# Optimization experiments

Measured on AMD Instinct MI355X. Metric: run time of the kernel, lower is better.

## Reference

```python
import jax, jax.numpy as jnp
import numpy as np

B, S, I, H, O = 32, 512, 512, 1024, 512

def setup_inputs() -> dict:
    key = jax.random.key(0)
    ks = jax.random.split(key, 11)
    sI = 1.0 / np.sqrt(I + H)
    sH = 1.0 / np.sqrt(H)
    return {
        "x": jax.random.normal(ks[0], (B, S, I), jnp.float32),
        "Wf_w": jax.random.normal(ks[1], (H, I + H), jnp.float32) * sI,
        "Wf_b": jax.random.normal(ks[2], (H,), jnp.float32) * sI,
        "Wi_w": jax.random.normal(ks[3], (H, I + H), jnp.float32) * sI,
        "Wi_b": jax.random.normal(ks[4], (H,), jnp.float32) * sI,
        "Wo_w": jax.random.normal(ks[5], (H, I + H), jnp.float32) * sI,
        "Wo_b": jax.random.normal(ks[6], (H,), jnp.float32) * sI,
        "Wc_w": jax.random.normal(ks[7], (H, I + H), jnp.float32) * sI,
        "Wc_b": jax.random.normal(ks[8], (H,), jnp.float32) * sI,
        "out_w": jax.random.normal(ks[9], (O, H), jnp.float32) * sH,
        "out_b": jax.random.normal(ks[10], (O,), jnp.float32) * sH,
    }

def reference(x, Wf_w, Wf_b, Wi_w, Wi_b, Wo_w, Wo_b, Wc_w, Wc_b, out_w, out_b):
    # Stack the 4 gate projections into one [4H, I+H] matmul per step (same math).
    W = jnp.concatenate([Wf_w, Wi_w, Wo_w, Wc_w], axis=0)          # [4H, I+H]
    b = jnp.concatenate([Wf_b, Wi_b, Wo_b, Wc_b], axis=0)          # [4H]
    Wx, Wh = W[:, :x.shape[-1]], W[:, x.shape[-1]:]                # split cat(x, h)
    # Precompute input contributions for all timesteps: [S, B, 4H]
    xg = jnp.einsum('bsi,gi->sbg', x, Wx) + b

    h0 = jnp.zeros((x.shape[0], Wh.shape[1]), x.dtype)
    c0 = jnp.zeros_like(h0)

    def step(carry, xg_t):
        h, c = carry
        g = xg_t + h @ Wh.T                                        # [B, 4H]
        f, i, o, chat = jnp.split(g, 4, axis=-1)
        f, i, o = jax.nn.sigmoid(f), jax.nn.sigmoid(i), jax.nn.sigmoid(o)
        c = f * c + i * jnp.tanh(chat)
        h = o * jnp.tanh(c)
        return (h, c), h

    (h_fin, c_fin), hs = jax.lax.scan(step, (h0, c0), xg)          # hs: [S, B, H]
    outputs = jnp.transpose(hs, (1, 0, 2))                         # [B, S, H]
    final = jnp.einsum('bsh,oh->bso', outputs, out_w) + out_b      # [B, S, O]
    return final, (h_fin, c_fin)
```

## Files before the change

kernel.cpp:

```cpp
#include <hip/hip_runtime.h>

typedef unsigned short u16;
typedef __attribute__((ext_vector_type(8))) short short8;
typedef __attribute__((ext_vector_type(4))) float f32x4;
typedef __attribute__((ext_vector_type(2))) float f32x2;

#define S_ 512
#define I_ 512
#define H_ 1024
#define B_ 32
#define G_ 4096
#define WROW 1536
#define CH_ 128
#define CHLOG_ 7
#define NREC 64
#define NWRK 192

__device__ __forceinline__ u16 f2b(float f){ union{float f;unsigned u;}c; c.f=f; unsigned u=c.u; return (u16)((u + 0x7FFFu + ((u>>16)&1u))>>16); }

__device__ __forceinline__ unsigned pk2(float a, float b){
  union{float f;unsigned u;} x, y; x.f=a; y.f=b;
  return (x.u>>16) | (y.u & 0xffff0000u);
}
__device__ __forceinline__ short8 cvt8(const float* __restrict__ p){
  f32x4 a = *(const f32x4*)p;
  f32x4 b = *(const f32x4*)(p+4);
  union{unsigned u[4]; short8 s;} r;
  r.u[0]=pk2(a[0],a[1]); r.u[1]=pk2(a[2],a[3]);
  r.u[2]=pk2(b[0],b[1]); r.u[3]=pk2(b[2],b[3]);
  return r.s;
}
__device__ __forceinline__ short8 cvt8r(f32x4 a, f32x4 b){
  union{unsigned u[4]; short8 s;} r;
  r.u[0]=pk2(a[0],a[1]); r.u[1]=pk2(a[2],a[3]);
  r.u[2]=pk2(b[0],b[1]); r.u[3]=pk2(b[2],b[3]);
  return r.s;
}
__device__ __forceinline__ f32x4 mfma16(short8 a, short8 b, f32x4 c){
  return __builtin_amdgcn_mfma_f32_16x16x32_bf16(a,b,c,0,0,0);
}
__device__ __forceinline__ float sigf(float x){ return 1.0f/(1.0f+__expf(-x)); }
__device__ __forceinline__ float tanhfast(float x){ return 1.0f - 2.0f/(__expf(2.0f*x)+1.0f); }

__global__ __launch_bounds__(256,2) void k_xg(
    const float* __restrict__ x,
    const float* __restrict__ Wf, const float* __restrict__ Wi,
    const float* __restrict__ Wo, const float* __restrict__ Wc,
    const float* __restrict__ bfp, const float* __restrict__ bip,
    const float* __restrict__ bop, const float* __restrict__ bcp,
    float* __restrict__ xg, int t0)
{
  const int gt = blockIdx.x;
  const int sg = blockIdx.y;
  const int wv = threadIdx.x>>6;
  const int ln = threadIdx.x&63;
  const int n16 = ln&15, qd = ln>>4;
  const int g0 = gt*64 + wv*16;
  const int q = g0>>10, j0 = g0&1023;
  const float* W  = (q==0)?Wf:(q==1)?Wi:(q==2)?Wo:Wc;
  const float* bb = (q==0)?bfp:(q==1)?bip:(q==2)?bop:bcp;

  short8 Bw[16];
  {
    const float* wr = W + (size_t)(j0+n16)*WROW + qd*8;
    #pragma unroll
    for(int kt=0;kt<16;++kt) Bw[kt] = cvt8(wr + kt*32);
  }
  const float bv = bb[j0+n16];

  for(int si=0; si<8; ++si){
    const int sl = sg*8 + si;
    const int s  = t0 + sl;
    const float* xp = x + (size_t)n16*(S_*I_) + (size_t)s*I_ + qd*8;
    f32x4 a0={0,0,0,0}, a1={0,0,0,0};
    #pragma unroll
    for(int kt=0;kt<16;++kt){
      short8 A0 = cvt8(xp + kt*32);
      short8 A1 = cvt8(xp + (size_t)16*(S_*I_) + kt*32);
      a0 = mfma16(A0, Bw[kt], a0);
      a1 = mfma16(A1, Bw[kt], a1);
    }
    float* op = xg + ((size_t)sl*G_ + g0 + n16)*B_ + qd*4;
    f32x4 o0, o1;
    #pragma unroll
    for(int r=0;r<4;++r){ o0[r]=a0[r]+bv; o1[r]=a1[r]+bv; }
    *(f32x4*)op = o0;
    *(f32x4*)(op+16) = o1;
  }
}

__global__ __launch_bounds__(256,2) void k_out(
  const u16* __restrict__ hs,
  const float* __restrict__ ow,
  const float* __restrict__ obp,
  float* __restrict__ out, int t0, int chlog)
{
  const int bst = blockIdx.x;
  const int ot  = blockIdx.y;
  const int wv = threadIdx.x>>6;
  const int ln = threadIdx.x&63;
  const int n16 = ln&15, qd = ln>>4;
  const int bs0 = bst*64 + wv*16 + n16;
  const u16* bp   = hs + (size_t)bs0*H_ + qd*8;
  const float* ap = ow + (size_t)(ot*64 + n16)*H_ + qd*8;
  f32x4 acc[4];
  #pragma unroll
  for(int m=0;m<4;++m) acc[m]=(f32x4){0.f,0.f,0.f,0.f};
  #pragma unroll 4
  for(int kt=0;kt<32;++kt){
    short8 Bfr = *(const short8*)(bp + kt*32);
    #pragma unroll
    for(int m=0;m<4;++m){
      short8 Afr = cvt8(ap + (size_t)m*16*H_ + kt*32);
      acc[m] = mfma16(Afr, Bfr, acc[m]);
    }
  }
  const int b  = bs0 >> chlog;
  const int sl = bs0 & ((1<<chlog)-1);
  float* orow = out + ((size_t)b*S_ + t0 + sl)*512;
  #pragma unroll
  for(int m=0;m<4;++m){
    const int o0 = ot*64 + m*16 + qd*4;
    f32x4 ov;
    #pragma unroll
    for(int r=0;r<4;++r) ov[r] = acc[m][r] + obp[o0+r];
    *(f32x4*)(orow + o0) = ov;
  }
}

__global__ __launch_bounds__(256,1) void k_fused(
  const float* __restrict__ x,
  const float* __restrict__ Wf, const float* __restrict__ Wi,
  const float* __restrict__ Wo, const float* __restrict__ Wc,
  const float* __restrict__ bfp, const float* __restrict__ bip,
  const float* __restrict__ bop, const float* __restrict__ bcp,
  const float* __restrict__ ow, const float* __restrict__ obp,
  const float* __restrict__ xg_cur,
  float* __restrict__ xg_next,
  const u16* __restrict__ hs_prev,
  u16* __restrict__ hs_cur,
  float* __restrict__ hfin, float* __restrict__ cfin,
  float* __restrict__ cbuf,
  unsigned* __restrict__ flags,
  float* __restrict__ out,
  int t0, int do_out)
{
  const int bid = blockIdx.x;
  const int tid = threadIdx.x;
  __shared__ float pbuf[4][4][16][38];

  if (bid < NREC){
    const int h0  = bid*16;
    const int kw  = tid>>6;
    const int ln  = tid&63;
    const int n16 = ln&15, qd = ln>>4;

    short8 Bf[4][8];
    {
      const int kcol = 512 + kw*256 + qd*8;
      const float* w0 = Wf + (size_t)(h0+n16)*WROW + kcol;
      const float* w1 = Wi + (size_t)(h0+n16)*WROW + kcol;
      const float* w2 = Wo + (size_t)(h0+n16)*WROW + kcol;
      const float* w3 = Wc + (size_t)(h0+n16)*WROW + kcol;
      #pragma unroll
      for(int k=0;k<8;++k){
        Bf[0][k] = cvt8(w0 + k*32);
        Bf[1][k] = cvt8(w1 + k*32);
        Bf[2][k] = cvt8(w2 + k*32);
        Bf[3][k] = cvt8(w3 + k*32);
      }
    }
    const int ub  = tid>>3;
    const int hi0 = (tid&7)*2;
    f32x2 c01 = *(const f32x2*)(cbuf + (size_t)ub*H_ + h0 + hi0);

    for(int tl=0; tl<CH_; ++tl){
      const int t = t0 + tl;
      float xv[2][4];
      {
        const float* xp = xg_cur + ((size_t)tl*G_ + h0 + hi0)*B_ + ub;
        #pragma unroll
        for(int q=0;q<4;++q){
          xv[0][q] = xp[(size_t)q*1024*B_];
          xv[1][q] = xp[(size_t)q*1024*B_ + B_];
        }
      }
      if (t>0){
        if (tid < 64){
          const unsigned goal = (unsigned)t;
          unsigned v;
          do {
            v = __hip_atomic_load(flags + (tid<<5), __ATOMIC_RELAXED, __HIP_MEMORY_SCOPE_AGENT);
            if (__ballot(v < goal) == 0ull) break;
            __builtin_amdgcn_s_sleep(1);
          } while (true);
        }
        __syncthreads();
      }
      const u16* hbase; size_t bstride;
      if (tl==0){ hbase = hs_prev + (size_t)(CH_-1)*H_; bstride = (size_t)CH_*H_; }
      else      { hbase = hs_cur  + (size_t)(tl-1)*H_;  bstride = (size_t)CH_*H_; }
      const int kcolq = kw*256 + qd*8;
      const u16* hp0 = hbase + (size_t)n16*bstride      + kcolq;
      const u16* hp1 = hbase + (size_t)(16+n16)*bstride + kcolq;
      short8 As0[8], As1[8];
      #pragma unroll
      for(int k=0;k<8;++k){
        As0[k] = *(const short8*)(hp0 + k*32);
        As1[k] = *(const short8*)(hp1 + k*32);
      }
      f32x4 acc[2][4];
      #pragma unroll
      for(int m=0;m<2;++m)
        #pragma unroll
        for(int q=0;q<4;++q) acc[m][q]=(f32x4){0.f,0.f,0.f,0.f};
      #pragma unroll
      for(int k=0;k<8;++k){
        #pragma unroll
        for(int q=0;q<4;++q){
          acc[0][q] = mfma16(As0[k], Bf[q][k], acc[0][q]);
          acc[1][q] = mfma16(As1[k], Bf[q][k], acc[1][q]);
        }
      }
      #pragma unroll
      for(int m=0;m<2;++m)
        #pragma unroll
        for(int q=0;q<4;++q){
          float* dst = &pbuf[kw][q][n16][m*16 + qd*4];
          *(f32x2*)dst       = (f32x2){acc[m][q][0], acc[m][q][1]};
          *(f32x2*)(dst + 2) = (f32x2){acc[m][q][2], acc[m][q][3]};
        }
      __syncthreads();
      float g[2][4];
      #pragma unroll
      for(int e=0;e<2;++e){
        #pragma unroll
        for(int q=0;q<4;++q){
          g[e][q] = xv[e][q] + pbuf[0][q][hi0+e][ub] + pbuf[1][q][hi0+e][ub]
                             + pbuf[2][q][hi0+e][ub] + pbuf[3][q][hi0+e][ub];
        }
      }
      float hv[2], cn[2];
      #pragma unroll
      for(int e=0;e<2;++e){
        float fg = sigf(g[e][0]);
        float ig = sigf(g[e][1]);
        float og = sigf(g[e][2]);
        float ch = tanhfast(g[e][3]);
        cn[e] = fg*c01[e] + ig*ch;
        hv[e] = og*tanhfast(cn[e]);
        c01[e] = cn[e];
      }
      const unsigned hpk = (unsigned)f2b(hv[0]) | ((unsigned)f2b(hv[1])<<16);
      unsigned* hw = (unsigned*)(hs_cur + ((size_t)ub*CH_ + tl)*H_ + h0 + hi0);
      __hip_atomic_store(hw, hpk, __ATOMIC_RELAXED, __HIP_MEMORY_SCOPE_AGENT);
      if (t==511){
        *(f32x2*)(hfin + (size_t)ub*H_ + h0 + hi0) = (f32x2){hv[0], hv[1]};
        *(f32x2*)(cfin + (size_t)ub*H_ + h0 + hi0) = (f32x2){cn[0], cn[1]};
      }
      if (tl==CH_-1)
        *(f32x2*)(cbuf + (size_t)ub*H_ + h0 + hi0) = c01;
      __syncthreads();
      if (tid==0)
        __hip_atomic_store(flags + (bid<<5), (unsigned)(t+1),
                           __ATOMIC_RELAXED, __HIP_MEMORY_SCOPE_AGENT);
    }
    return;
  }

  const int w  = bid - NREC;
  const int wv = tid>>6;
  const int ln = tid&63;
  const int n16 = ln&15, qd = ln>>4;

  if (xg_next){
    const int gt = w & 63;
    const int g0 = gt*64 + wv*16;
    const int q = g0>>10, j0 = g0&1023;
    const float* W  = (q==0)?Wf:(q==1)?Wi:(q==2)?Wo:Wc;
    const float* bb = (q==0)?bfp:(q==1)?bip:(q==2)?bop:bcp;
    short8 Bw[16];
    {
      const float* wr = W + (size_t)(j0+n16)*WROW + qd*8;
      #pragma unroll
      for(int kt=0;kt<16;++kt) Bw[kt] = cvt8(wr + kt*32);
    }
    const float bv = bb[j0+n16];
    for (int sg = w>>6; sg < 16; sg += 3){
      for(int si=0; si<8; ++si){
        const int sl = sg*8 + si;
        const int s  = t0 + CH_ + sl;
        const float* xp = x + (size_t)n16*(S_*I_) + (size_t)s*I_ + qd*8;
        f32x4 a0={0,0,0,0}, a1={0,0,0,0};
        #pragma unroll
        for(int h=0;h<2;++h){
          f32x4 pa[8][2], pb[8][2];
          #pragma unroll
          for(int k8=0;k8<8;++k8){
            const int kt = h*8 + k8;
            pa[k8][0] = *(const f32x4*)(xp + kt*32);
            pa[k8][1] = *(const f32x4*)(xp + kt*32 + 4);
            pb[k8][0] = *(const f32x4*)(xp + (size_t)16*(S_*I_) + kt*32);
            pb[k8][1] = *(const f32x4*)(xp + (size_t)16*(S_*I_) + kt*32 + 4);
          }
          #pragma unroll
          for(int k8=0;k8<8;++k8){
            const int kt = h*8 + k8;
            a0 = mfma16(cvt8r(pa[k8][0], pa[k8][1]), Bw[kt], a0);
            a1 = mfma16(cvt8r(pb[k8][0], pb[k8][1]), Bw[kt], a1);
          }
        }
        float* op = xg_next + ((size_t)sl*G_ + g0 + n16)*B_ + qd*4;
        f32x4 o0, o1;
        #pragma unroll
        for(int r=0;r<4;++r){ o0[r]=a0[r]+bv; o1[r]=a1[r]+bv; }
        *(f32x4*)op = o0;
        *(f32x4*)(op+16) = o1;
      }
    }
  }

  if (do_out){
    for (int tau = w; tau < 512; tau += NWRK){
      const int bst = tau & 63, ot = tau >> 6;
      const int bs0 = bst*64 + wv*16 + n16;
      const u16* bp   = hs_prev + (size_t)bs0*H_ + qd*8;
      const float* ap = ow + (size_t)(ot*64 + n16)*H_ + qd*8;
      f32x4 acc[4];
      #pragma unroll
      for(int m=0;m<4;++m) acc[m]=(f32x4){0.f,0.f,0.f,0.f};
      #pragma unroll
      for(int g=0;g<8;++g){
        short8 hbf[4];
        f32x4 wa[4][4][2];
        #pragma unroll
        for(int k4=0;k4<4;++k4){
          const int kt = g*4 + k4;
          hbf[k4] = *(const short8*)(bp + kt*32);
          #pragma unroll
          for(int m=0;m<4;++m){
            wa[k4][m][0] = *(const f32x4*)(ap + (size_t)m*16*H_ + kt*32);
            wa[k4][m][1] = *(const f32x4*)(ap + (size_t)m*16*H_ + kt*32 + 4);
          }
        }
        #pragma unroll
        for(int k4=0;k4<4;++k4)
          #pragma unroll
          for(int m=0;m<4;++m)
            acc[m] = mfma16(cvt8r(wa[k4][m][0], wa[k4][m][1]), hbf[k4], acc[m]);
      }
      const int b  = bs0 >> CHLOG_;
      const int sl = bs0 & (CH_-1);
      float* orow = out + ((size_t)b*S_ + (t0 - CH_) + sl)*512;
      #pragma unroll
      for(int m=0;m<4;++m){
        const int o0 = ot*64 + m*16 + qd*4;
        f32x4 ov;
        #pragma unroll
        for(int r=0;r<4;++r) ov[r] = acc[m][r] + obp[o0+r];
        *(f32x4*)(orow + o0) = ov;
      }
    }
  }
}

extern "C" void kernel_launch(void* const* d_in, const int* in_sizes, int n_in,
                              void* d_out, int out_size, void* d_ws, size_t ws_size,
                              hipStream_t stream)
{
  const float* x  = (const float*)d_in[0];
  const float* Wf = (const float*)d_in[1];
  const float* bf = (const float*)d_in[2];
  const float* Wi = (const float*)d_in[3];
  const float* bi = (const float*)d_in[4];
  const float* Wo = (const float*)d_in[5];
  const float* bo = (const float*)d_in[6];
  const float* Wc = (const float*)d_in[7];
  const float* bc = (const float*)d_in[8];
  const float* ow = (const float*)d_in[9];
  const float* ob = (const float*)d_in[10];
  float* out = (float*)d_out;

  char* ws = (char*)d_ws;
  unsigned* flags = (unsigned*)ws;
  float* cbuf  = (float*)(ws + 8192);
  u16*   hsb[2] = { (u16*)(ws + 139264), (u16*)(ws + 8527872) };
  float* xgb[2] = { (float*)(ws + 16916480), (float*)(ws + 84025344) };
  float* hfin = out + (size_t)8388608;
  float* cfin = out + (size_t)8421376;

  hipMemsetAsync(ws, 0, 16916480, stream);

  k_xg<<<dim3(64, CH_/8), 256, 0, stream>>>(x, Wf, Wi, Wo, Wc, bf, bi, bo, bc, xgb[0], 0);

  for(int c=0; c<4; ++c){
    const float* a_xgc = xgb[c&1];
    float*       a_xgn = (c<3) ? xgb[(c+1)&1] : (float*)0;
    const u16*   a_hsp = hsb[(c+1)&1];
    u16*         a_hsc = hsb[c&1];
    int a_t0 = c*CH_;
    int a_do = (c>0) ? 1 : 0;
    void* args[] = { (void*)&x,
                     (void*)&Wf, (void*)&Wi, (void*)&Wo, (void*)&Wc,
                     (void*)&bf, (void*)&bi, (void*)&bo, (void*)&bc,
                     (void*)&ow, (void*)&ob,
                     (void*)&a_xgc, (void*)&a_xgn, (void*)&a_hsp, (void*)&a_hsc,
                     (void*)&hfin, (void*)&cfin, (void*)&cbuf, (void*)&flags,
                     (void*)&out, (void*)&a_t0, (void*)&a_do };
    hipLaunchCooperativeKernel((const void*)k_fused, dim3(NREC+NWRK), dim3(256), args, 0, stream);
  }

  k_out<<<dim3(CH_/2, 8), 256, 0, stream>>>(hsb[1], ow, ob, out, 3*CH_, CHLOG_);
}
```

Measured before the change: 2.836 ms.

## Replace per-step flag barrier with sentinel-valued h data polling

Removes the per-timestep flag array that each recurrent block published and polled before reading h. Consumers now load the bf16 h fragments directly and spin only on words that still hold a 0xFFFFFFFF sentinel, so synchronisation rides on the data itself. The h buffers are pre-filled with the sentinel by memsets before each chunk. This cuts one global round-trip and a block-wide barrier per step, at the cost of extra memset traffic and reliance on a packed bf16 pair never equalling the sentinel. It also depends on 32-bit stores becoming visible without relying on release ordering.

```diff
diff --git a/kernel.cpp b/kernel.cpp
--- a/kernel.cpp
+++ b/kernel.cpp
@@ -15,6 +15,7 @@
 #define CHLOG_ 7
 #define NREC 64
 #define NWRK 192
+#define SENT 0xFFFFFFFFu
 
 __device__ __forceinline__ u16 f2b(float f){ union{float f;unsigned u;}c; c.f=f; unsigned u=c.u; return (u16)((u + 0x7FFFu + ((u>>16)&1u))>>16); }
 
@@ -141,7 +142,6 @@
   u16* __restrict__ hs_cur,
   float* __restrict__ hfin, float* __restrict__ cfin,
   float* __restrict__ cbuf,
-  unsigned* __restrict__ flags,
   float* __restrict__ out,
   int t0, int do_out)
 {
@@ -185,29 +185,45 @@
           xv[1][q] = xp[(size_t)q*1024*B_ + B_];
         }
       }
-      if (t>0){
-        if (tid < 64){
-          const unsigned goal = (unsigned)t;
-          unsigned v;
-          do {
-            v = __hip_atomic_load(flags + (tid<<5), __ATOMIC_RELAXED, __HIP_MEMORY_SCOPE_AGENT);
-            if (__ballot(v < goal) == 0ull) break;
-            __builtin_amdgcn_s_sleep(1);
-          } while (true);
-        }
-        __syncthreads();
-      }
       const u16* hbase; size_t bstride;
       if (tl==0){ hbase = hs_prev + (size_t)(CH_-1)*H_; bstride = (size_t)CH_*H_; }
       else      { hbase = hs_cur  + (size_t)(tl-1)*H_;  bstride = (size_t)CH_*H_; }
       const int kcolq = kw*256 + qd*8;
       const u16* hp0 = hbase + (size_t)n16*bstride      + kcolq;
       const u16* hp1 = hbase + (size_t)(16+n16)*bstride + kcolq;
-      short8 As0[8], As1[8];
+      union Frag { short8 s; unsigned u[4]; };
+      Frag As0[8], As1[8];
       #pragma unroll
       for(int k=0;k<8;++k){
-        As0[k] = *(const short8*)(hp0 + k*32);
-        As1[k] = *(const short8*)(hp1 + k*32);
+        As0[k].s = *(const short8*)(hp0 + k*32);
+        As1[k].s = *(const short8*)(hp1 + k*32);
+      }
+      if (t>0){
+        bool bad = false;
+        #pragma unroll
+        for(int k=0;k<8;++k){
+          #pragma unroll
+          for(int j=0;j<4;++j)
+            bad = bad | (As0[k].u[j]==SENT) | (As1[k].u[j]==SENT);
+        }
+        if (__builtin_expect(__ballot(bad) != 0ull, 0)){
+          #pragma unroll
+          for(int k=0;k<8;++k){
+            const unsigned* g0 = (const unsigned*)(hp0 + k*32);
+            const unsigned* g1 = (const unsigned*)(hp1 + k*32);
+            #pragma unroll
+            for(int j=0;j<4;++j){
+              while (As0[k].u[j]==SENT){
+                __builtin_amdgcn_s_sleep(1);
+                As0[k].u[j] = __hip_atomic_load(g0+j, __ATOMIC_RELAXED, __HIP_MEMORY_SCOPE_AGENT);
+              }
+              while (As1[k].u[j]==SENT){
+                __builtin_amdgcn_s_sleep(1);
+                As1[k].u[j] = __hip_atomic_load(g1+j, __ATOMIC_RELAXED, __HIP_MEMORY_SCOPE_AGENT);
+              }
+            }
+          }
+        }
       }
       f32x4 acc[2][4];
       #pragma unroll
@@ -218,8 +234,8 @@
       for(int k=0;k<8;++k){
         #pragma unroll
         for(int q=0;q<4;++q){
-          acc[0][q] = mfma16(As0[k], Bf[q][k], acc[0][q]);
-          acc[1][q] = mfma16(As1[k], Bf[q][k], acc[1][q]);
+          acc[0][q] = mfma16(As0[k].s, Bf[q][k], acc[0][q]);
+          acc[1][q] = mfma16(As1[k].s, Bf[q][k], acc[1][q]);
         }
       }
       #pragma unroll
@@ -261,9 +277,6 @@
       if (tl==CH_-1)
         *(f32x2*)(cbuf + (size_t)ub*H_ + h0 + hi0) = c01;
       __syncthreads();
-      if (tid==0)
-        __hip_atomic_store(flags + (bid<<5), (unsigned)(t+1),
-                           __ATOMIC_RELAXED, __HIP_MEMORY_SCOPE_AGENT);
     }
     return;
   }
@@ -382,18 +395,21 @@
   float* out = (float*)d_out;
 
   char* ws = (char*)d_ws;
-  unsigned* flags = (unsigned*)ws;
   float* cbuf  = (float*)(ws + 8192);
   u16*   hsb[2] = { (u16*)(ws + 139264), (u16*)(ws + 8527872) };
   float* xgb[2] = { (float*)(ws + 16916480), (float*)(ws + 84025344) };
   float* hfin = out + (size_t)8388608;
   float* cfin = out + (size_t)8421376;
 
-  hipMemsetAsync(ws, 0, 16916480, stream);
+  hipMemsetAsync(ws, 0, 139264, stream);
+  hipMemsetAsync(ws + 139264, 0xFF, 8388608, stream);
+  hipMemsetAsync(ws + 8527872, 0, 8388608, stream);
 
   k_xg<<<dim3(64, CH_/8), 256, 0, stream>>>(x, Wf, Wi, Wo, Wc, bf, bi, bo, bc, xgb[0], 0);
 
   for(int c=0; c<4; ++c){
+    if (c >= 1)
+      hipMemsetAsync((void*)hsb[c&1], 0xFF, 8388608, stream);
     const float* a_xgc = xgb[c&1];
     float*       a_xgn = (c<3) ? xgb[(c+1)&1] : (float*)0;
     const u16*   a_hsp = hsb[(c+1)&1];
@@ -405,7 +421,7 @@
                      (void*)&bf, (void*)&bi, (void*)&bo, (void*)&bc,
                      (void*)&ow, (void*)&ob,
                      (void*)&a_xgc, (void*)&a_xgn, (void*)&a_hsp, (void*)&a_hsc,
-                     (void*)&hfin, (void*)&cfin, (void*)&cbuf, (void*)&flags,
+                     (void*)&hfin, (void*)&cfin, (void*)&cbuf,
                      (void*)&out, (void*)&a_t0, (void*)&a_do };
     hipLaunchCooperativeKernel((const void*)k_fused, dim3(NREC+NWRK), dim3(256), args, 0, stream);
   }
```

Measured after the change: 7.276 ms. +156.6%, slower.
